# Kernel optimization log

Hardware: AMD Instinct MI355X
Metric: run time of the kernel (lower is better)

## Reference

```python
import jax, jax.numpy as jnp
import numpy as np

B, H, W = 16, 128, 128
NUM_SAMPLES, HID = 16, 256


def setup_inputs() -> dict:
    key = jax.random.key(0)
    ks = jax.random.split(key, 12)
    inp = {
        "x": jax.random.uniform(ks[0], (B, H, W, 2), jnp.float32) * 2.0 - 1.0,
        "sample_idx": jax.random.randint(ks[1], (B,), 0, NUM_SAMPLES),
        "shift_vectors": jax.random.normal(ks[2], (NUM_SAMPLES, 2), jnp.float32) * 0.05,
        "rotation_angle": jax.random.normal(ks[3], (NUM_SAMPLES, 1), jnp.float32) * 0.05,
        "color_scales": 1.0 + jax.random.normal(ks[4], (NUM_SAMPLES, 3), jnp.float32) * 0.05,
        "color_shifts": jax.random.normal(ks[5], (NUM_SAMPLES, 3), jnp.float32) * 0.05,
        "W1": jax.random.normal(ks[6], (2, HID), jnp.float32) / np.sqrt(2.0),
        "b1": jnp.zeros((HID,), jnp.float32),
        "W2": jax.random.normal(ks[7], (HID, HID), jnp.float32) / np.sqrt(HID),
        "b2": jnp.zeros((HID,), jnp.float32),
        "W3": jax.random.normal(ks[8], (HID, HID), jnp.float32) / np.sqrt(HID),
        "b3": jnp.zeros((HID,), jnp.float32),
        "W4": jax.random.normal(ks[9], (HID, 3), jnp.float32) / np.sqrt(HID),
        "b4": jnp.zeros((3,), jnp.float32),
    }
    return inp


def reference(x, sample_idx, shift_vectors, rotation_angle, color_scales, color_shifts,
              W1, b1, W2, b2, W3, b3, W4, b4):
    # Per-sample affine coordinate transform (vectorized gather + batched 2x3 affine).
    shift = shift_vectors[sample_idx]            # [B,2] -> (dy, dx)
    dy, dx = shift[:, 0], shift[:, 1]
    ang = rotation_angle[sample_idx, 0]          # [B]
    c, s = jnp.cos(ang), jnp.sin(ang)
    rot = jnp.stack([jnp.stack([c, -s], -1),
                     jnp.stack([s, c], -1)], -2)  # [B,2,2]
    trans = jnp.stack([dx, dy], -1)               # [B,2]
    coords = jnp.einsum('bij,bhwj->bhwi', rot, x) + trans[:, None, None, :]

    # INR decoder MLP: coords -> RGB
    h = jax.nn.relu(coords @ W1 + b1)
    h = jax.nn.relu(h @ W2 + b2)
    h = jax.nn.relu(h @ W3 + b3)
    out = h @ W4 + b4                             # [B,H,W,3]

    # Per-sample color affine, skipped for reference sample idx==0.
    scales = color_scales[sample_idx][:, None, None, :]
    shifts = color_shifts[sample_idx][:, None, None, :]
    mask = (sample_idx != 0)[:, None, None, None]
    out = jnp.where(mask, out * scales + shifts, out)
    return out, dx, dy
```

## Files before the change

### kernel.cpp

```cpp
#include <hip/hip_runtime.h>
#include <math.h>

typedef _Float16 half8  __attribute__((ext_vector_type(8)));
typedef _Float16 half4v __attribute__((ext_vector_type(4)));
typedef _Float16 half2v __attribute__((ext_vector_type(2)));
typedef float    f32x4  __attribute__((ext_vector_type(4)));

#define W1OFF 0
#define W2OFF 8192
#define W3OFF 73728
#define W4OFF 139264
#define SWTOT 143360
#define OUT_PIX (16*128*128)

__global__ void inr_prep(const float* __restrict__ W1, const float* __restrict__ W2,
                         const float* __restrict__ W3, const float* __restrict__ W4,
                         const int* __restrict__ sidx, const float* __restrict__ sv,
                         _Float16* __restrict__ wsw, float* __restrict__ outtail)
{
    int tid = blockIdx.x * 256 + threadIdx.x;
    if (tid < 16) {
        int si = sidx[tid];
        outtail[tid]      = sv[2*si + 1];
        outtail[16 + tid] = sv[2*si + 0];
    }
    if (tid >= SWTOT) return;
    int kind, rel;
    if      (tid < W2OFF) { kind = 0; rel = tid; }
    else if (tid < W3OFF) { kind = 1; rel = tid - W2OFF; }
    else if (tid < W4OFF) { kind = 2; rel = tid - W3OFF; }
    else                  { kind = 3; rel = tid - W4OFF; }
    int j    = rel & 7;
    int lane = (rel >> 3) & 63;
    int blk  = rel >> 9;
    int q = lane >> 4, ln = lane & 15;
    float val;
    if (kind == 3) {
        int m = ln;
        int k = blk * 32 + q * 8 + j;
        val = (m < 3) ? W4[k*3 + m] : 0.0f;
    } else {
        int MT = blk & 15, kkb = blk >> 4;
        int m = MT*16 + ln;
        int k = kkb*32 + q*8 + j;
        if      (kind == 0) val = (k < 2) ? W1[k*256 + m] : 0.0f;
        else if (kind == 1) val = W2[k*256 + m];
        else                val = W3[k*256 + m];
    }
    wsw[tid] = (_Float16)val;
}

template<int NKK>
__device__ __forceinline__ void do_layer(const half8* __restrict__ Asw,
                                         const float* __restrict__ bias,
                                         _Float16* hbuf, int w, int q, int ln, int lane)
{
    f32x4 acc[4][8];
#pragma unroll
    for (int mt = 0; mt < 4; ++mt)
#pragma unroll
        for (int nt = 0; nt < 8; ++nt)
            acc[mt][nt] = (f32x4){0.f, 0.f, 0.f, 0.f};

#pragma unroll
    for (int kkb = 0; kkb < NKK; ++kkb) {
        half8 aw[4];
#pragma unroll
        for (int mt = 0; mt < 4; ++mt)
            aw[mt] = Asw[(kkb*16 + 4*w + mt)*64 + lane];
        half8 bf[8];
        int g = kkb*4 + q;
#pragma unroll
        for (int nt = 0; nt < 8; ++nt)
            bf[nt] = *(const half8*)&hbuf[g*1024 + (16*nt + ln)*8];
#pragma unroll
        for (int nt = 0; nt < 8; ++nt)
#pragma unroll
            for (int mt = 0; mt < 4; ++mt)
                acc[mt][nt] = __builtin_amdgcn_mfma_f32_16x16x32_f16(aw[mt], bf[nt], acc[mt][nt], 0, 0, 0);
    }
    __syncthreads();
#pragma unroll
    for (int mt = 0; mt < 4; ++mt) {
        int hid0 = 64*w + 16*mt + 4*q;
        f32x4 bv = *(const f32x4*)&bias[hid0];
        int g = hid0 >> 3;
        int o = hid0 & 7;
#pragma unroll
        for (int nt = 0; nt < 8; ++nt) {
            int pixel = 16*nt + ln;
            f32x4 a = acc[mt][nt];
            half4v hv;
            hv[0] = (_Float16)fmaxf(a[0] + bv[0], 0.f);
            hv[1] = (_Float16)fmaxf(a[1] + bv[1], 0.f);
            hv[2] = (_Float16)fmaxf(a[2] + bv[2], 0.f);
            hv[3] = (_Float16)fmaxf(a[3] + bv[3], 0.f);
            *(half4v*)&hbuf[g*1024 + pixel*8 + o] = hv;
        }
    }
    __syncthreads();
}

__launch_bounds__(256, 2)
__global__ void inr_fused(const float* __restrict__ x, const int* __restrict__ sidx_p,
                          const float* __restrict__ sv, const float* __restrict__ ra,
                          const float* __restrict__ cs, const float* __restrict__ csh,
                          const float* __restrict__ b1, const float* __restrict__ b2,
                          const float* __restrict__ b3, const float* __restrict__ b4,
                          const _Float16* __restrict__ wsw, float* __restrict__ out)
{
    __shared__ __align__(16) _Float16 hbuf[32768];
    int t = threadIdx.x;
    int lane = t & 63, w = t >> 6, q = lane >> 4, ln = lane & 15;
    int pixbase = blockIdx.x * 128;
    int b = pixbase >> 14;
    int sidx = sidx_p[b];
    float dy = sv[2*sidx], dx = sv[2*sidx + 1];
    float ang = ra[sidx];
    float sn, cn;
    sincosf(ang, &sn, &cn);

    if (t < 128) {
        int p = t;
        float x0 = x[(pixbase + p)*2 + 0];
        float x1 = x[(pixbase + p)*2 + 1];
        float u = cn*x0 - sn*x1 + dx;
        float v = sn*x0 + cn*x1 + dy;
        half8 z;
#pragma unroll
        for (int i = 0; i < 8; ++i) z[i] = (_Float16)0.0f;
#pragma unroll
        for (int g = 1; g < 4; ++g)
            *(half8*)&hbuf[g*1024 + p*8] = z;
        z[0] = (_Float16)u; z[1] = (_Float16)v;
        *(half8*)&hbuf[0*1024 + p*8] = z;
    }
    __syncthreads();

    const half8* wsw8 = (const half8*)wsw;
    do_layer<1>(wsw8,                b1, hbuf, w, q, ln, lane);
    do_layer<8>(wsw8 + (W2OFF >> 3), b2, hbuf, w, q, ln, lane);
    do_layer<8>(wsw8 + (W3OFF >> 3), b3, hbuf, w, q, ln, lane);

    const half8* w4p = wsw8 + (W4OFF >> 3);
    f32x4 a4[2];
    a4[0] = (f32x4){0.f,0.f,0.f,0.f};
    a4[1] = (f32x4){0.f,0.f,0.f,0.f};
#pragma unroll
    for (int kkb = 0; kkb < 8; ++kkb) {
        half8 aw = w4p[kkb*64 + lane];
#pragma unroll
        for (int i = 0; i < 2; ++i) {
            int pixel = 16*(2*w + i) + ln;
            half8 bf = *(const half8*)&hbuf[(kkb*4 + q)*1024 + pixel*8];
            a4[i] = __builtin_amdgcn_mfma_f32_16x16x32_f16(aw, bf, a4[i], 0, 0, 0);
        }
    }
    if (q == 0) {
        bool doc = (sidx != 0);
        float s0 = cs[sidx*3+0], s1 = cs[sidx*3+1], s2 = cs[sidx*3+2];
        float t0 = csh[sidx*3+0], t1 = csh[sidx*3+1], t2 = csh[sidx*3+2];
        float bb0 = b4[0], bb1 = b4[1], bb2 = b4[2];
#pragma unroll
        for (int i = 0; i < 2; ++i) {
            int gp = pixbase + 16*(2*w + i) + ln;
            float v0 = a4[i][0] + bb0;
            float v1 = a4[i][1] + bb1;
            float v2 = a4[i][2] + bb2;
            if (doc) { v0 = v0*s0 + t0; v1 = v1*s1 + t1; v2 = v2*s2 + t2; }
            out[gp*3 + 0] = v0;
            out[gp*3 + 1] = v1;
            out[gp*3 + 2] = v2;
        }
    }
}

extern "C" void kernel_launch(void* const* d_in, const int* in_sizes, int n_in,
                              void* d_out, int out_size, void* d_ws, size_t ws_size,
                              hipStream_t stream)
{
    const float* x    = (const float*)d_in[0];
    const int*   sidx = (const int*)  d_in[1];
    const float* sv   = (const float*)d_in[2];
    const float* ra   = (const float*)d_in[3];
    const float* cs   = (const float*)d_in[4];
    const float* csh  = (const float*)d_in[5];
    const float* W1   = (const float*)d_in[6];
    const float* b1   = (const float*)d_in[7];
    const float* W2   = (const float*)d_in[8];
    const float* b2   = (const float*)d_in[9];
    const float* W3   = (const float*)d_in[10];
    const float* b3   = (const float*)d_in[11];
    const float* W4   = (const float*)d_in[12];
    const float* b4   = (const float*)d_in[13];
    float* out = (float*)d_out;
    _Float16* wsw = (_Float16*)d_ws;

    inr_prep<<<SWTOT/256, 256, 0, stream>>>(W1, W2, W3, W4, sidx, sv, wsw, out + OUT_PIX*3);
    inr_fused<<<OUT_PIX/128, 256, 0, stream>>>(x, sidx, sv, ra, cs, csh,
                                               b1, b2, b3, b4, wsw, out);
}
```

Before: 144.3 us.

## Prefetch next layer weights across barriers and use lgkm-only barriers

Each layer's first k-block of weights is prefetched into registers before the barrier ahead of it, so the global load overlaps the bias/ReLU epilogue and the sync. __syncthreads is replaced with a barrier that waits only on LDS counters, so outstanding global prefetches are not drained. MFMA loops raise wave priority, the bias/ReLU conversion moves ahead of the barrier, and the zero-fill of hbuf is split across both halves of the block with a vectorized x load. This adds register pressure under launch bounds of 2 blocks per CU, which risks spills.

Measured after the change: 143.3 us. No clear change (-0.7%).

```diff
diff --git a/kernel.cpp b/kernel.cpp
--- a/kernel.cpp
+++ b/kernel.cpp
@@ -3,8 +3,8 @@
 
 typedef _Float16 half8  __attribute__((ext_vector_type(8)));
 typedef _Float16 half4v __attribute__((ext_vector_type(4)));
-typedef _Float16 half2v __attribute__((ext_vector_type(2)));
 typedef float    f32x4  __attribute__((ext_vector_type(4)));
+typedef float    f32x2  __attribute__((ext_vector_type(2)));
 
 #define W1OFF 0
 #define W2OFF 8192
@@ -50,10 +50,21 @@
     wsw[tid] = (_Float16)val;
 }
 
-template<int NKK>
+__device__ __forceinline__ void lgkm_barrier()
+{
+    __builtin_amdgcn_sched_barrier(0);
+    asm volatile("s_waitcnt lgkmcnt(0)" ::: "memory");
+    __builtin_amdgcn_s_barrier();
+    __builtin_amdgcn_sched_barrier(0);
+}
+
+template<int NKK, int NNEXT>
 __device__ __forceinline__ void do_layer(const half8* __restrict__ Asw,
                                          const float* __restrict__ bias,
-                                         _Float16* hbuf, int w, int q, int ln, int lane)
+                                         _Float16* hbuf, int w, int q, int ln, int lane,
+                                         const half8 (&awpre)[4],
+                                         const half8* __restrict__ nextAw,
+                                         half8 (&awnext)[4])
 {
     f32x4 acc[4][8];
 #pragma unroll
@@ -62,12 +73,14 @@
         for (int nt = 0; nt < 8; ++nt)
             acc[mt][nt] = (f32x4){0.f, 0.f, 0.f, 0.f};
 
+    __builtin_amdgcn_s_setprio(1);
 #pragma unroll
     for (int kkb = 0; kkb < NKK; ++kkb) {
         half8 aw[4];
 #pragma unroll
         for (int mt = 0; mt < 4; ++mt)
-            aw[mt] = Asw[(kkb*16 + 4*w + mt)*64 + lane];
+            aw[mt] = (kkb == 0) ? awpre[mt]
+                                : Asw[(kkb*16 + 4*w + mt)*64 + lane];
         half8 bf[8];
         int g = kkb*4 + q;
 #pragma unroll
@@ -79,26 +92,39 @@
             for (int mt = 0; mt < 4; ++mt)
                 acc[mt][nt] = __builtin_amdgcn_mfma_f32_16x16x32_f16(aw[mt], bf[nt], acc[mt][nt], 0, 0, 0);
     }
-    __syncthreads();
+    __builtin_amdgcn_s_setprio(0);
+
+    half4v hv[4][8];
 #pragma unroll
     for (int mt = 0; mt < 4; ++mt) {
         int hid0 = 64*w + 16*mt + 4*q;
         f32x4 bv = *(const f32x4*)&bias[hid0];
+#pragma unroll
+        for (int nt = 0; nt < 8; ++nt) {
+            f32x4 a = acc[mt][nt];
+            half4v h;
+            h[0] = (_Float16)fmaxf(a[0] + bv[0], 0.f);
+            h[1] = (_Float16)fmaxf(a[1] + bv[1], 0.f);
+            h[2] = (_Float16)fmaxf(a[2] + bv[2], 0.f);
+            h[3] = (_Float16)fmaxf(a[3] + bv[3], 0.f);
+            hv[mt][nt] = h;
+        }
+    }
+#pragma unroll
+    for (int mt = 0; mt < NNEXT; ++mt)
+        awnext[mt] = nextAw[mt*64 + lane];
+
+    lgkm_barrier();
+#pragma unroll
+    for (int mt = 0; mt < 4; ++mt) {
+        int hid0 = 64*w + 16*mt + 4*q;
         int g = hid0 >> 3;
         int o = hid0 & 7;
 #pragma unroll
-        for (int nt = 0; nt < 8; ++nt) {
-            int pixel = 16*nt + ln;
-            f32x4 a = acc[mt][nt];
-            half4v hv;
-            hv[0] = (_Float16)fmaxf(a[0] + bv[0], 0.f);
-            hv[1] = (_Float16)fmaxf(a[1] + bv[1], 0.f);
-            hv[2] = (_Float16)fmaxf(a[2] + bv[2], 0.f);
-            hv[3] = (_Float16)fmaxf(a[3] + bv[3], 0.f);
-            *(half4v*)&hbuf[g*1024 + pixel*8 + o] = hv;
-        }
-    }
-    __syncthreads();
+        for (int nt = 0; nt < 8; ++nt)
+            *(half4v*)&hbuf[g*1024 + (16*nt + ln)*8 + o] = hv[mt][nt];
+    }
+    lgkm_barrier();
 }
 
 __launch_bounds__(256, 2)
@@ -115,6 +141,13 @@
     int pixbase = blockIdx.x * 128;
     int b = pixbase >> 14;
     int sidx = sidx_p[b];
+
+    const half8* wsw8 = (const half8*)wsw;
+    half8 awA[4], awB[4];
+#pragma unroll
+    for (int mt = 0; mt < 4; ++mt)
+        awA[mt] = wsw8[(4*w + mt)*64 + lane];
+
     float dy = sv[2*sidx], dx = sv[2*sidx + 1];
     float ang = ra[sidx];
     float sn, cn;
@@ -122,33 +155,40 @@
 
     if (t < 128) {
         int p = t;
-        float x0 = x[(pixbase + p)*2 + 0];
-        float x1 = x[(pixbase + p)*2 + 1];
-        float u = cn*x0 - sn*x1 + dx;
-        float v = sn*x0 + cn*x1 + dy;
+        f32x2 xv = *(const f32x2*)&x[(pixbase + p)*2];
+        float u = cn*xv[0] - sn*xv[1] + dx;
+        float v = sn*xv[0] + cn*xv[1] + dy;
         half8 z;
 #pragma unroll
         for (int i = 0; i < 8; ++i) z[i] = (_Float16)0.0f;
-#pragma unroll
-        for (int g = 1; g < 4; ++g)
-            *(half8*)&hbuf[g*1024 + p*8] = z;
         z[0] = (_Float16)u; z[1] = (_Float16)v;
         *(half8*)&hbuf[0*1024 + p*8] = z;
-    }
-    __syncthreads();
-
-    const half8* wsw8 = (const half8*)wsw;
-    do_layer<1>(wsw8,                b1, hbuf, w, q, ln, lane);
-    do_layer<8>(wsw8 + (W2OFF >> 3), b2, hbuf, w, q, ln, lane);
-    do_layer<8>(wsw8 + (W3OFF >> 3), b3, hbuf, w, q, ln, lane);
+    } else {
+        int p = t - 128;
+        half8 z;
+#pragma unroll
+        for (int i = 0; i < 8; ++i) z[i] = (_Float16)0.0f;
+        *(half8*)&hbuf[1*1024 + p*8] = z;
+        *(half8*)&hbuf[2*1024 + p*8] = z;
+        *(half8*)&hbuf[3*1024 + p*8] = z;
+    }
+    lgkm_barrier();
+
+    do_layer<1,4>(wsw8,               b1, hbuf, w, q, ln, lane, awA,
+                  wsw8 + (W2OFF>>3) + (4*w)*64, awB);
+    do_layer<8,4>(wsw8 + (W2OFF>>3),  b2, hbuf, w, q, ln, lane, awB,
+                  wsw8 + (W3OFF>>3) + (4*w)*64, awA);
+    do_layer<8,1>(wsw8 + (W3OFF>>3),  b3, hbuf, w, q, ln, lane, awA,
+                  wsw8 + (W4OFF>>3),            awB);
 
     const half8* w4p = wsw8 + (W4OFF >> 3);
     f32x4 a4[2];
     a4[0] = (f32x4){0.f,0.f,0.f,0.f};
     a4[1] = (f32x4){0.f,0.f,0.f,0.f};
+    __builtin_amdgcn_s_setprio(1);
 #pragma unroll
     for (int kkb = 0; kkb < 8; ++kkb) {
-        half8 aw = w4p[kkb*64 + lane];
+        half8 aw = (kkb == 0) ? awB[0] : w4p[kkb*64 + lane];
 #pragma unroll
         for (int i = 0; i < 2; ++i) {
             int pixel = 16*(2*w + i) + ln;
@@ -156,6 +196,8 @@
             a4[i] = __builtin_amdgcn_mfma_f32_16x16x32_f16(aw, bf, a4[i], 0, 0, 0);
         }
     }
+    __builtin_amdgcn_s_setprio(0);
+
     if (q == 0) {
         bool doc = (sidx != 0);
         float s0 = cs[sidx*3+0], s1 = cs[sidx*3+1], s2 = cs[sidx*3+2];
```

## Switch hidden-layer MFMAs from 16x16x32 to 32x32x16 tiles

Applied to the files above, without the earlier changes.

Rewrites the three hidden layers to use 32x32x16 f16 MFMA instructions. Each wave now computes 2x4 tiles of 32x32 instead of 4x8 tiles of 16x16, and the prep kernel's weight swizzle is changed to match. The first layer's padded K shrinks from 32 to 16, so only one zero group needs to be written into the shared buffer. Larger tiles mean fewer A/B fragment loads from LDS per FLOP. The risks are different register pressure and different LDS bank patterns in the write-back.

After: 144.9 us. No clear change (+0.4%).

```diff
diff --git a/kernel.cpp b/kernel.cpp
--- a/kernel.cpp
+++ b/kernel.cpp
@@ -3,14 +3,15 @@
 
 typedef _Float16 half8  __attribute__((ext_vector_type(8)));
 typedef _Float16 half4v __attribute__((ext_vector_type(4)));
-typedef _Float16 half2v __attribute__((ext_vector_type(2)));
 typedef float    f32x4  __attribute__((ext_vector_type(4)));
+typedef float    f32x2  __attribute__((ext_vector_type(2)));
+typedef float    f32x16 __attribute__((ext_vector_type(16)));
 
 #define W1OFF 0
-#define W2OFF 8192
-#define W3OFF 73728
-#define W4OFF 139264
-#define SWTOT 143360
+#define W2OFF 4096
+#define W3OFF 69632
+#define W4OFF 135168
+#define SWTOT 139264
 #define OUT_PIX (16*128*128)
 
 __global__ void inr_prep(const float* __restrict__ W1, const float* __restrict__ W2,
@@ -33,69 +34,78 @@
     int j    = rel & 7;
     int lane = (rel >> 3) & 63;
     int blk  = rel >> 9;
-    int q = lane >> 4, ln = lane & 15;
     float val;
     if (kind == 3) {
+        int q = lane >> 4, ln = lane & 15;
         int m = ln;
         int k = blk * 32 + q * 8 + j;
         val = (m < 3) ? W4[k*3 + m] : 0.0f;
     } else {
-        int MT = blk & 15, kkb = blk >> 4;
-        int m = MT*16 + ln;
-        int k = kkb*32 + q*8 + j;
-        if      (kind == 0) val = (k < 2) ? W1[k*256 + m] : 0.0f;
-        else if (kind == 1) val = W2[k*256 + m];
-        else                val = W3[k*256 + m];
+        int hi = lane >> 5, lo = lane & 31;
+        if (kind == 0) {
+            int m = blk*32 + lo;
+            int k = hi*8 + j;
+            val = (k < 2) ? W1[k*256 + m] : 0.0f;
+        } else {
+            int MT = blk & 7, kk = blk >> 3;
+            int m = MT*32 + lo;
+            int k = kk*16 + hi*8 + j;
+            val = (kind == 1) ? W2[k*256 + m] : W3[k*256 + m];
+        }
     }
     wsw[tid] = (_Float16)val;
 }
 
 template<int NKK>
-__device__ __forceinline__ void do_layer(const half8* __restrict__ Asw,
-                                         const float* __restrict__ bias,
-                                         _Float16* hbuf, int w, int q, int ln, int lane)
-{
-    f32x4 acc[4][8];
-#pragma unroll
-    for (int mt = 0; mt < 4; ++mt)
-#pragma unroll
-        for (int nt = 0; nt < 8; ++nt)
-            acc[mt][nt] = (f32x4){0.f, 0.f, 0.f, 0.f};
-
-#pragma unroll
-    for (int kkb = 0; kkb < NKK; ++kkb) {
-        half8 aw[4];
-#pragma unroll
-        for (int mt = 0; mt < 4; ++mt)
-            aw[mt] = Asw[(kkb*16 + 4*w + mt)*64 + lane];
-        half8 bf[8];
-        int g = kkb*4 + q;
-#pragma unroll
-        for (int nt = 0; nt < 8; ++nt)
-            bf[nt] = *(const half8*)&hbuf[g*1024 + (16*nt + ln)*8];
-#pragma unroll
-        for (int nt = 0; nt < 8; ++nt)
-#pragma unroll
-            for (int mt = 0; mt < 4; ++mt)
-                acc[mt][nt] = __builtin_amdgcn_mfma_f32_16x16x32_f16(aw[mt], bf[nt], acc[mt][nt], 0, 0, 0);
+__device__ __forceinline__ void do_layer32(const half8* __restrict__ Asw,
+                                           const float* __restrict__ bias,
+                                           _Float16* hbuf, int w, int lane)
+{
+    int lo = lane & 31, hi = lane >> 5;
+    f32x16 acc[2][4];
+#pragma unroll
+    for (int mt = 0; mt < 2; ++mt)
+#pragma unroll
+        for (int nt = 0; nt < 4; ++nt)
+#pragma unroll
+            for (int r = 0; r < 16; ++r)
+                acc[mt][nt][r] = 0.f;
+
+#pragma unroll
+    for (int kk = 0; kk < NKK; ++kk) {
+        half8 aw[2];
+#pragma unroll
+        for (int mt = 0; mt < 2; ++mt)
+            aw[mt] = Asw[(kk*8 + 2*w + mt)*64 + lane];
+        half8 bf[4];
+        int g = kk*2 + hi;
+#pragma unroll
+        for (int nt = 0; nt < 4; ++nt)
+            bf[nt] = *(const half8*)&hbuf[g*1024 + (32*nt + lo)*8];
+#pragma unroll
+        for (int nt = 0; nt < 4; ++nt)
+#pragma unroll
+            for (int mt = 0; mt < 2; ++mt)
+                acc[mt][nt] = __builtin_amdgcn_mfma_f32_32x32x16_f16(aw[mt], bf[nt], acc[mt][nt], 0, 0, 0);
     }
     __syncthreads();
 #pragma unroll
-    for (int mt = 0; mt < 4; ++mt) {
-        int hid0 = 64*w + 16*mt + 4*q;
-        f32x4 bv = *(const f32x4*)&bias[hid0];
-        int g = hid0 >> 3;
-        int o = hid0 & 7;
-#pragma unroll
-        for (int nt = 0; nt < 8; ++nt) {
-            int pixel = 16*nt + ln;
-            f32x4 a = acc[mt][nt];
-            half4v hv;
-            hv[0] = (_Float16)fmaxf(a[0] + bv[0], 0.f);
-            hv[1] = (_Float16)fmaxf(a[1] + bv[1], 0.f);
-            hv[2] = (_Float16)fmaxf(a[2] + bv[2], 0.f);
-            hv[3] = (_Float16)fmaxf(a[3] + bv[3], 0.f);
-            *(half4v*)&hbuf[g*1024 + pixel*8 + o] = hv;
+    for (int mt = 0; mt < 2; ++mt) {
+        int MT = 2*w + mt;
+#pragma unroll
+        for (int gi = 0; gi < 4; ++gi) {
+            int hid0 = MT*32 + gi*8 + 4*hi;
+            f32x4 bv = *(const f32x4*)&bias[hid0];
+#pragma unroll
+            for (int nt = 0; nt < 4; ++nt) {
+                int px = 32*nt + lo;
+                half4v hv;
+                hv[0] = (_Float16)fmaxf(acc[mt][nt][gi*4+0] + bv[0], 0.f);
+                hv[1] = (_Float16)fmaxf(acc[mt][nt][gi*4+1] + bv[1], 0.f);
+                hv[2] = (_Float16)fmaxf(acc[mt][nt][gi*4+2] + bv[2], 0.f);
+                hv[3] = (_Float16)fmaxf(acc[mt][nt][gi*4+3] + bv[3], 0.f);
+                *(half4v*)&hbuf[(MT*4 + gi)*1024 + px*8 + 4*hi] = hv;
+            }
         }
     }
     __syncthreads();
@@ -122,25 +132,27 @@
 
     if (t < 128) {
         int p = t;
-        float x0 = x[(pixbase + p)*2 + 0];
-        float x1 = x[(pixbase + p)*2 + 1];
-        float u = cn*x0 - sn*x1 + dx;
-        float v = sn*x0 + cn*x1 + dy;
+        f32x2 xv = *(const f32x2*)&x[(pixbase + p)*2];
+        float u = cn*xv[0] - sn*xv[1] + dx;
+        float v = sn*xv[0] + cn*xv[1] + dy;
         half8 z;
 #pragma unroll
         for (int i = 0; i < 8; ++i) z[i] = (_Float16)0.0f;
-#pragma unroll
-        for (int g = 1; g < 4; ++g)
-            *(half8*)&hbuf[g*1024 + p*8] = z;
         z[0] = (_Float16)u; z[1] = (_Float16)v;
         *(half8*)&hbuf[0*1024 + p*8] = z;
+    } else {
+        int p = t - 128;
+        half8 z;
+#pragma unroll
+        for (int i = 0; i < 8; ++i) z[i] = (_Float16)0.0f;
+        *(half8*)&hbuf[1*1024 + p*8] = z;
     }
     __syncthreads();
 
     const half8* wsw8 = (const half8*)wsw;
-    do_layer<1>(wsw8,                b1, hbuf, w, q, ln, lane);
-    do_layer<8>(wsw8 + (W2OFF >> 3), b2, hbuf, w, q, ln, lane);
-    do_layer<8>(wsw8 + (W3OFF >> 3), b3, hbuf, w, q, ln, lane);
+    do_layer32<1>(wsw8,                b1, hbuf, w, lane);
+    do_layer32<16>(wsw8 + (W2OFF >> 3), b2, hbuf, w, lane);
+    do_layer32<16>(wsw8 + (W3OFF >> 3), b3, hbuf, w, lane);
 
     const half8* w4p = wsw8 + (W4OFF >> 3);
     f32x4 a4[2];
```
